# Optimization experiments

Measured on AMD Instinct MI355X. Metric: run time of the kernel, lower is better.

Reference implementation:

```python
import jax, jax.numpy as jnp
import numpy as np

B, S, HID = 4, 1024, 1024
NH, HD = 16, 64  # num heads, head dim


def setup_inputs() -> dict:
    key = jax.random.key(0)
    ks = jax.random.split(key, 8)
    scale = 0.02
    return {
        "hidden_states": jax.random.normal(ks[0], (B, S, HID), dtype=jnp.float32),
        "attention_mask": jnp.ones((B, 1, 1, S), dtype=jnp.float32),
        "Wq": jax.random.normal(ks[1], (HID, HID), dtype=jnp.float32) * scale,
        "bq": jnp.zeros((HID,), dtype=jnp.float32),
        "Wk": jax.random.normal(ks[2], (HID, HID), dtype=jnp.float32) * scale,
        "bk": jnp.zeros((HID,), dtype=jnp.float32),
        "Wv": jax.random.normal(ks[3], (HID, HID), dtype=jnp.float32) * scale,
        "bv": jnp.zeros((HID,), dtype=jnp.float32),
    }


def reference(hidden_states, attention_mask, Wq, bq, Wk, bk, Wv, bv):
    # Linear projections: torch nn.Linear computes x @ W.T + b
    q = hidden_states @ Wq.T + bq  # [B,S,HID]
    k = hidden_states @ Wk.T + bk
    v = hidden_states @ Wv.T + bv

    def split_heads(x):
        return x.reshape(B, S, NH, HD).transpose(0, 2, 1, 3)  # [B,NH,S,HD]

    q, k, v = split_heads(q), split_heads(k), split_heads(v)

    scores = jnp.einsum("bhqd,bhkd->bhqk", q, k) / jnp.sqrt(jnp.float32(HD))
    # faithful to original: scores - (2 - mask) * 1e6
    scores = scores - (2.0 - attention_mask) * 1.0e6
    probs = jax.nn.softmax(scores, axis=-1)
    # dropout: eval mode -> identity
    ctx = jnp.einsum("bhqk,bhkd->bhqd", probs, v)  # [B,NH,S,HD]
    ctx = ctx.transpose(0, 2, 1, 3).reshape(B, S, HID)
    return ctx
```

## Files before the change

### kernel.cpp

```cpp
#include <hip/hip_runtime.h>
#include <math.h>

#define B_ 4
#define S_ 1024
#define HID_ 1024
#define NH_ 16
#define HD_ 64
#define NTOK (B_ * S_)

typedef __attribute__((ext_vector_type(4))) float f32x4;
typedef __attribute__((ext_vector_type(8))) short bf16x8;

__device__ __forceinline__ unsigned short f2bf(float f) {
    union { float f; unsigned int u; } v; v.f = f;
    unsigned int r = v.u + 0x7fffu + ((v.u >> 16) & 1u);
    return (unsigned short)(r >> 16);
}

#if __has_builtin(__builtin_amdgcn_cvt_pk_bf16_f32)
__device__ __forceinline__ unsigned int pk_bf16(float a, float b) {
    auto v = __builtin_amdgcn_cvt_pk_bf16_f32(a, b);
    union { decltype(v) v; unsigned int u; } cv; cv.v = v;
    return cv.u;
}
#else
__device__ __forceinline__ unsigned int pk_bf16(float a, float b) {
    return (unsigned int)f2bf(a) | ((unsigned int)f2bf(b) << 16);
}
#endif

__device__ __forceinline__ void load_lds16(const void* g, void* l) {
    __builtin_amdgcn_global_load_lds(
        (const __attribute__((address_space(1))) unsigned int*)(uintptr_t)g,
        (__attribute__((address_space(3))) unsigned int*)(uintptr_t)l,
        16, 0, 0);
}

__global__ __launch_bounds__(256) void cvt_all(
    const float* __restrict__ x, const float* __restrict__ wq,
    const float* __restrict__ wk, const float* __restrict__ wv,
    unsigned short* __restrict__ xb, unsigned short* __restrict__ wqb,
    unsigned short* __restrict__ wkb, unsigned short* __restrict__ wvb)
{
    const int which = blockIdx.y;
    const float* src = which == 0 ? x : which == 1 ? wq : which == 2 ? wk : wv;
    unsigned short* dst = which == 0 ? xb : which == 1 ? wqb : which == 2 ? wkb : wvb;
    const int n4 = (which == 0) ? (NTOK * HID_ / 4) : (HID_ * HID_ / 4);
    int i = blockIdx.x * 256 + threadIdx.x;
    if (i < n4) {
        float4 f = ((const float4*)src)[i];
        uint2 o;
        o.x = pk_bf16(f.x, f.y);
        o.y = pk_bf16(f.z, f.w);
        ((uint2*)dst)[i] = o;
    }
}

__global__ __launch_bounds__(512, 6) void qkv_gemm_mfma(
    const unsigned short* __restrict__ xb,
    const unsigned short* __restrict__ Wqb, const float* __restrict__ bq,
    const unsigned short* __restrict__ Wkb, const float* __restrict__ bk,
    const unsigned short* __restrict__ Wvb, const float* __restrict__ bv,
    unsigned short* __restrict__ qout, unsigned short* __restrict__ kout,
    unsigned short* __restrict__ vtout)
{
    const int which = blockIdx.z;
    const unsigned short* __restrict__ W = which == 0 ? Wqb : which == 1 ? Wkb : Wvb;
    const float* __restrict__ bias       = which == 0 ? bq  : which == 1 ? bk  : bv;

    __shared__ unsigned short As[128 * 64];
    __shared__ unsigned short Bs[128 * 64];

    const int t    = threadIdx.x;
    const int lane = t & 63;
    const int w    = t >> 6;
    const int wr   = w >> 2;
    const int wc   = w & 3;
    const int g    = lane >> 4;
    const int lrow = lane & 15;

    const int bm = blockIdx.x;
    const int bn = blockIdx.y;

    const unsigned short* __restrict__ Arow = (which == 2) ? W  : xb;
    const unsigned short* __restrict__ Brow = (which == 2) ? xb : W;
    const int am0 = (which == 2) ? bn * 128 : bm * 128;
    const int bn0 = (which == 2) ? bm * 128 : bn * 128;

    const int srow = t >> 3;
    const int sc   = ((t & 7) ^ ((t >> 3) & 7)) << 3;
    const unsigned short* gA = Arow + (size_t)(am0 + srow) * HID_ + sc;
    const unsigned short* gB = Brow + (size_t)(bn0 + srow) * HID_ + sc;

    const f32x4 zero = {0.f, 0.f, 0.f, 0.f};
    f32x4 acc[4][2];
    #pragma unroll
    for (int i = 0; i < 4; ++i)
        #pragma unroll
        for (int j = 0; j < 2; ++j) acc[i][j] = zero;

    for (int k0 = 0; k0 < HID_; k0 += 64) {
        __syncthreads();
        #pragma unroll
        for (int i = 0; i < 2; ++i) {
            load_lds16(gA + (size_t)(i * 64) * HID_ + k0, (char*)As + i * 8192 + t * 16);
            load_lds16(gB + (size_t)(i * 64) * HID_ + k0, (char*)Bs + i * 8192 + t * 16);
        }
        __syncthreads();

        #pragma unroll
        for (int ks = 0; ks < 2; ++ks) {
            bf16x8 af[4], bf[2];
            #pragma unroll
            for (int i = 0; i < 4; ++i) {
                const int row = wr * 64 + i * 16 + lrow;
                af[i] = *(const bf16x8*)&As[row * 64 + (((ks * 4 + g) ^ (row & 7)) << 3)];
            }
            #pragma unroll
            for (int j = 0; j < 2; ++j) {
                const int row = wc * 32 + j * 16 + lrow;
                bf[j] = *(const bf16x8*)&Bs[row * 64 + (((ks * 4 + g) ^ (row & 7)) << 3)];
            }
            #pragma unroll
            for (int i = 0; i < 4; ++i)
                #pragma unroll
                for (int j = 0; j < 2; ++j)
                    acc[i][j] = __builtin_amdgcn_mfma_f32_16x16x32_bf16(
                        af[i], bf[j], acc[i][j], 0, 0, 0);
        }
    }

    const int col   = lane & 15;
    const int rbase = (lane >> 4) << 2;
    if (which == 2) {
        #pragma unroll
        for (int i = 0; i < 4; ++i) {
            #pragma unroll
            for (int r = 0; r < 4; ++r) {
                const int feat = bn * 128 + wr * 64 + i * 16 + rbase + r;
                const int h = feat >> 6, d = feat & 63;
                const float bias_v = bias[feat];
                #pragma unroll
                for (int j = 0; j < 2; ++j) {
                    const int tok = bm * 128 + wc * 32 + j * 16 + col;
                    const int b = tok >> 10, s = tok & 1023;
                    vtout[((size_t)((b << 4) + h) << 16) + ((size_t)d << 10) + s] =
                        f2bf(acc[i][j][r] + bias_v);
                }
            }
        }
    } else {
        #pragma unroll
        for (int j = 0; j < 2; ++j) {
            const int feat = bn * 128 + wc * 32 + j * 16 + col;
            const int h = feat >> 6, d = feat & 63;
            const float bias_v = bias[feat];
            #pragma unroll
            for (int i = 0; i < 4; ++i) {
                const int tok0 = bm * 128 + wr * 64 + i * 16 + rbase;
                #pragma unroll
                for (int r = 0; r < 4; ++r) {
                    const int tok = tok0 + r;
                    const int b = tok >> 10, s = tok & 1023;
                    const size_t off = ((size_t)((b << 4) + h) << 16) + ((size_t)s << 6) + d;
                    const float val = acc[i][j][r] + bias_v;
                    if (which == 0) qout[off] = f2bf(val);
                    else            kout[off] = f2bf(val);
                }
            }
        }
    }
}

__global__ __launch_bounds__(512, 4) void attn_mfma(
    const unsigned short* __restrict__ Q, const unsigned short* __restrict__ K,
    const unsigned short* __restrict__ Vt, const float* __restrict__ mask,
    float* __restrict__ out)
{
    __shared__ unsigned short Ks[2][64 * 64];
    __shared__ unsigned short Vts[2][64 * 64];
    __shared__ unsigned short Ps[8][16 * 72];
    __shared__ float Mts[1024];
    __shared__ float Ls[8][16];

    const int t    = threadIdx.x;
    const int lane = t & 63;
    const int w    = t >> 6;
    const int g    = lane >> 4;
    const int ln   = lane & 15;

    const int bh = blockIdx.x;
    const int b  = bh >> 4;
    const int h  = bh & 15;
    const int q0 = blockIdx.y << 7;

    const unsigned short* __restrict__ qg = Q  + ((size_t)bh << 16);
    const unsigned short* __restrict__ kg = K  + ((size_t)bh << 16);
    const unsigned short* __restrict__ vg = Vt + ((size_t)bh << 16);

    const int qrow = w * 16 + ln;

    bf16x8 qreg[2];
    #pragma unroll
    for (int ks = 0; ks < 2; ++ks)
        qreg[ks] = *(const bf16x8*)&qg[(size_t)(q0 + qrow) * 64 + ks * 32 + (g << 3)];

    int fro[2][4];
    #pragma unroll
    for (int ks = 0; ks < 2; ++ks)
        #pragma unroll
        for (int j = 0; j < 4; ++j) {
            const int row = j * 16 + ln;
            fro[ks][j] = (row * 64 + (((ks * 4 + g) ^ (row & 7)) << 3)) * 2;
        }

    const int srow = t >> 3;
    const int scol = ((t & 7) ^ (srow & 7)) << 3;
    const unsigned short* kst = kg + (size_t)srow * 64 + scol;
    const unsigned short* vst = vg + (size_t)srow * 1024 + scol;

    const f32x4 zero = {0.f, 0.f, 0.f, 0.f};
    f32x4 O[4];
    #pragma unroll
    for (int j = 0; j < 4; ++j) O[j] = zero;
    float lacc = 0.f;

    load_lds16(kst, (char*)Ks[0] + t * 16);
    load_lds16(vst, (char*)Vts[0] + t * 16);
    #pragma unroll
    for (int i = 0; i < 2; ++i) {
        const int key = t + i * 512;
        Mts[key] = (2.0f - mask[(b << 10) + key]) * 1.0e6f;
    }
    __syncthreads();

    for (int kt = 0; kt < 16; ++kt) {
        const int cur = kt & 1;

        if (kt < 15) {
            load_lds16(kst + (size_t)(kt + 1) * 4096, (char*)Ks[cur ^ 1] + t * 16);
            load_lds16(vst + (size_t)(kt + 1) * 64,  (char*)Vts[cur ^ 1] + t * 16);
        }

        const unsigned short* Kb = Ks[cur];
        const unsigned short* Vb = Vts[cur];

        f32x4 sacc[4];
        #pragma unroll
        for (int j = 0; j < 4; ++j) sacc[j] = zero;
        {
            bf16x8 kf[2][4];
            #pragma unroll
            for (int ks = 0; ks < 2; ++ks)
                #pragma unroll
                for (int j = 0; j < 4; ++j)
                    kf[ks][j] = *(const bf16x8*)((const char*)Kb + fro[ks][j]);
            __builtin_amdgcn_s_setprio(1);
            #pragma unroll
            for (int ks = 0; ks < 2; ++ks)
                #pragma unroll
                for (int j = 0; j < 4; ++j)
                    sacc[j] = __builtin_amdgcn_mfma_f32_16x16x32_bf16(
                        kf[ks][j], qreg[ks], sacc[j], 0, 0, 0);
            __builtin_amdgcn_s_setprio(0);
        }

        #pragma unroll
        for (int j = 0; j < 4; ++j) {
            const f32x4 m4 = *(const f32x4*)&Mts[kt * 64 + j * 16 + (g << 2)];
            float p[4];
            #pragma unroll
            for (int r = 0; r < 4; ++r) {
                const float sv = sacc[j][r] * 0.125f - m4[r];
                p[r] = __expf(sv + 1.0e6f);
            }
            lacc += (p[0] + p[1]) + (p[2] + p[3]);
            uint2 pk;
            pk.x = pk_bf16(p[0], p[1]);
            pk.y = pk_bf16(p[2], p[3]);
            *(uint2*)&Ps[w][ln * 72 + j * 16 + (g << 2)] = pk;
        }
        asm volatile("s_waitcnt lgkmcnt(0)" ::: "memory");

        {
            bf16x8 pf[2], vf[2][4];
            #pragma unroll
            for (int ks = 0; ks < 2; ++ks) {
                pf[ks] = *(const bf16x8*)&Ps[w][ln * 72 + ks * 32 + (g << 3)];
                #pragma unroll
                for (int j = 0; j < 4; ++j)
                    vf[ks][j] = *(const bf16x8*)((const char*)Vb + fro[ks][j]);
            }
            __builtin_amdgcn_s_setprio(1);
            #pragma unroll
            for (int ks = 0; ks < 2; ++ks)
                #pragma unroll
                for (int j = 0; j < 4; ++j)
                    O[j] = __builtin_amdgcn_mfma_f32_16x16x32_bf16(
                        pf[ks], vf[ks][j], O[j], 0, 0, 0);
            __builtin_amdgcn_s_setprio(0);
        }

        __syncthreads();
    }

    float rs = lacc;
    rs += __shfl_xor(rs, 16);
    rs += __shfl_xor(rs, 32);
    if (lane < 16) Ls[w][ln] = rs;
    asm volatile("s_waitcnt lgkmcnt(0)" ::: "memory");
    #pragma unroll
    for (int r = 0; r < 4; ++r) {
        const float inv = 1.0f / Ls[w][(g << 2) + r];
        const int q = q0 + w * 16 + (g << 2) + r;
        const size_t base = (((size_t)(b << 10) + q) << 10) + (h << 6);
        #pragma unroll
        for (int j = 0; j < 4; ++j)
            out[base + j * 16 + ln] = O[j][r] * inv;
    }
}

extern "C" void kernel_launch(void* const* d_in, const int* in_sizes, int n_in,
                              void* d_out, int out_size, void* d_ws, size_t ws_size,
                              hipStream_t stream) {
    const float* hs   = (const float*)d_in[0];
    const float* mask = (const float*)d_in[1];
    const float* Wq   = (const float*)d_in[2];
    const float* bq   = (const float*)d_in[3];
    const float* Wk   = (const float*)d_in[4];
    const float* bk   = (const float*)d_in[5];
    const float* Wv   = (const float*)d_in[6];
    const float* bv   = (const float*)d_in[7];
    float* out = (float*)d_out;

    char* ws = (char*)d_ws;
    unsigned short* xb  = (unsigned short*)(ws);
    unsigned short* wqb = (unsigned short*)(ws + ((size_t)8  << 20));
    unsigned short* wkb = (unsigned short*)(ws + ((size_t)10 << 20));
    unsigned short* wvb = (unsigned short*)(ws + ((size_t)12 << 20));
    unsigned short* qb  = (unsigned short*)(ws + ((size_t)14 << 20));
    unsigned short* kb  = (unsigned short*)(ws + ((size_t)22 << 20));
    unsigned short* vtb = (unsigned short*)(ws + ((size_t)30 << 20));

    cvt_all<<<dim3(4096, 4), 256, 0, stream>>>(hs, Wq, Wk, Wv, xb, wqb, wkb, wvb);
    qkv_gemm_mfma<<<dim3(NTOK / 128, HID_ / 128, 3), 512, 0, stream>>>(
        xb, wqb, bq, wkb, bk, wvb, bv, qb, kb, vtb);
    attn_mfma<<<dim3(B_ * NH_, S_ / 128), 512, 0, stream>>>(qb, kb, vtb, mask, out);
}
```

Before: 148.1 us.

## Switch attention to 32x32x16 MFMA with register-resident P via permlane swaps

```diff
diff --git a/kernel.cpp b/kernel.cpp
--- a/kernel.cpp
+++ b/kernel.cpp
@@ -9,6 +9,7 @@
 #define NTOK (B_ * S_)
 
 typedef __attribute__((ext_vector_type(4))) float f32x4;
+typedef __attribute__((ext_vector_type(16))) float f32x16;
 typedef __attribute__((ext_vector_type(8))) short bf16x8;
 
 __device__ __forceinline__ unsigned short f2bf(float f) {
@@ -26,6 +27,23 @@
 #else
 __device__ __forceinline__ unsigned int pk_bf16(float a, float b) {
     return (unsigned int)f2bf(a) | ((unsigned int)f2bf(b) << 16);
+}
+#endif
+
+#if __has_builtin(__builtin_amdgcn_permlane32_swap)
+__device__ __forceinline__ void plswap(unsigned &a, unsigned &b) {
+    typedef __attribute__((ext_vector_type(2))) int v2i;
+    v2i r = __builtin_amdgcn_permlane32_swap((int)a, (int)b, false, false);
+    a = (unsigned)r[0]; b = (unsigned)r[1];
+}
+#else
+__device__ __forceinline__ void plswap(unsigned &a, unsigned &b) {
+    const unsigned bl = __shfl_xor(b, 32);
+    const unsigned ah = __shfl_xor(a, 32);
+    const bool hi = ((threadIdx.x & 63) >> 5) != 0;
+    const unsigned na = hi ? bl : a;
+    const unsigned nb = hi ? b  : ah;
+    a = na; b = nb;
 }
 #endif
 
@@ -172,64 +190,62 @@
     }
 }
 
-__global__ __launch_bounds__(512, 4) void attn_mfma(
+__global__ __launch_bounds__(256, 2) void attn_mfma(
     const unsigned short* __restrict__ Q, const unsigned short* __restrict__ K,
     const unsigned short* __restrict__ Vt, const float* __restrict__ mask,
     float* __restrict__ out)
 {
     __shared__ unsigned short Ks[2][64 * 64];
     __shared__ unsigned short Vts[2][64 * 64];
-    __shared__ unsigned short Ps[8][16 * 72];
     __shared__ float Mts[1024];
-    __shared__ float Ls[8][16];
+    __shared__ float Ls[4][32];
 
     const int t    = threadIdx.x;
     const int lane = t & 63;
     const int w    = t >> 6;
-    const int g    = lane >> 4;
-    const int ln   = lane & 15;
+    const int q31  = lane & 31;
+    const int hl   = lane >> 5;
 
     const int bh = blockIdx.x;
     const int b  = bh >> 4;
     const int h  = bh & 15;
-    const int q0 = blockIdx.y << 7;
+    const int q0w = (blockIdx.y << 7) + (w << 5);
 
     const unsigned short* __restrict__ qg = Q  + ((size_t)bh << 16);
     const unsigned short* __restrict__ kg = K  + ((size_t)bh << 16);
     const unsigned short* __restrict__ vg = Vt + ((size_t)bh << 16);
 
-    const int qrow = w * 16 + ln;
-
-    bf16x8 qreg[2];
-    #pragma unroll
-    for (int ks = 0; ks < 2; ++ks)
-        qreg[ks] = *(const bf16x8*)&qg[(size_t)(q0 + qrow) * 64 + ks * 32 + (g << 3)];
-
-    int fro[2][4];
-    #pragma unroll
-    for (int ks = 0; ks < 2; ++ks)
-        #pragma unroll
-        for (int j = 0; j < 4; ++j) {
-            const int row = j * 16 + ln;
-            fro[ks][j] = (row * 64 + (((ks * 4 + g) ^ (row & 7)) << 3)) * 2;
-        }
+    bf16x8 qreg[4];
+    {
+        const unsigned short* qp = qg + ((size_t)(q0w + q31) << 6);
+        #pragma unroll
+        for (int kc = 0; kc < 4; ++kc)
+            qreg[kc] = *(const bf16x8*)&qp[kc * 16 + (hl << 3)];
+    }
+
+    int fro[4];
+    #pragma unroll
+    for (int kc = 0; kc < 4; ++kc)
+        fro[kc] = q31 * 128 + ((((kc << 1) + hl) ^ (q31 & 7)) << 4);
 
     const int srow = t >> 3;
-    const int scol = ((t & 7) ^ (srow & 7)) << 3;
-    const unsigned short* kst = kg + (size_t)srow * 64 + scol;
-    const unsigned short* vst = vg + (size_t)srow * 1024 + scol;
-
-    const f32x4 zero = {0.f, 0.f, 0.f, 0.f};
-    f32x4 O[4];
-    #pragma unroll
-    for (int j = 0; j < 4; ++j) O[j] = zero;
+    const int c8   = ((t & 7) ^ (srow & 7)) << 3;
+    const unsigned short* kst = kg + (size_t)srow * 64 + c8;
+    const unsigned short* vst = vg + (size_t)srow * 1024 + c8;
+
+    f32x16 O[2];
+    #pragma unroll
+    for (int i = 0; i < 16; ++i) { O[0][i] = 0.f; O[1][i] = 0.f; }
     float lacc = 0.f;
 
-    load_lds16(kst, (char*)Ks[0] + t * 16);
-    load_lds16(vst, (char*)Vts[0] + t * 16);
     #pragma unroll
     for (int i = 0; i < 2; ++i) {
-        const int key = t + i * 512;
+        load_lds16(kst + i * 2048,  (char*)Ks[0]  + i * 4096 + t * 16);
+        load_lds16(vst + i * 32768, (char*)Vts[0] + i * 4096 + t * 16);
+    }
+    #pragma unroll
+    for (int i = 0; i < 4; ++i) {
+        const int key = t + i * 256;
         Mts[key] = (2.0f - mask[(b << 10) + key]) * 1.0e6f;
     }
     __syncthreads();
@@ -238,85 +254,91 @@
         const int cur = kt & 1;
 
         if (kt < 15) {
-            load_lds16(kst + (size_t)(kt + 1) * 4096, (char*)Ks[cur ^ 1] + t * 16);
-            load_lds16(vst + (size_t)(kt + 1) * 64,  (char*)Vts[cur ^ 1] + t * 16);
-        }
-
-        const unsigned short* Kb = Ks[cur];
-        const unsigned short* Vb = Vts[cur];
-
-        f32x4 sacc[4];
-        #pragma unroll
-        for (int j = 0; j < 4; ++j) sacc[j] = zero;
-        {
-            bf16x8 kf[2][4];
-            #pragma unroll
-            for (int ks = 0; ks < 2; ++ks)
+            #pragma unroll
+            for (int i = 0; i < 2; ++i) {
+                load_lds16(kst + i * 2048 + (size_t)(kt + 1) * 4096,
+                           (char*)Ks[cur ^ 1] + i * 4096 + t * 16);
+                load_lds16(vst + i * 32768 + (size_t)(kt + 1) * 64,
+                           (char*)Vts[cur ^ 1] + i * 4096 + t * 16);
+            }
+        }
+
+        const char* Kb = (const char*)Ks[cur];
+        const char* Vb = (const char*)Vts[cur];
+
+        f32x16 sacc[2];
+        #pragma unroll
+        for (int i = 0; i < 16; ++i) { sacc[0][i] = 0.f; sacc[1][i] = 0.f; }
+        #pragma unroll
+        for (int kb = 0; kb < 2; ++kb) {
+            bf16x8 kf[4];
+            #pragma unroll
+            for (int kc = 0; kc < 4; ++kc)
+                kf[kc] = *(const bf16x8*)(Kb + kb * 4096 + fro[kc]);
+            __builtin_amdgcn_s_setprio(1);
+            #pragma unroll
+            for (int kc = 0; kc < 4; ++kc)
+                sacc[kb] = __builtin_amdgcn_mfma_f32_32x32x16_bf16(
+                    kf[kc], qreg[kc], sacc[kb], 0, 0, 0);
+            __builtin_amdgcn_s_setprio(0);
+        }
+
+        bf16x8 pf[4];
+        #pragma unroll
+        for (int kb = 0; kb < 2; ++kb) {
+            unsigned u[4][2];
+            #pragma unroll
+            for (int rq = 0; rq < 4; ++rq) {
+                const f32x4 m4 = *(const f32x4*)&Mts[kt * 64 + kb * 32 + rq * 8 + (hl << 2)];
+                float p[4];
                 #pragma unroll
-                for (int j = 0; j < 4; ++j)
-                    kf[ks][j] = *(const bf16x8*)((const char*)Kb + fro[ks][j]);
+                for (int r = 0; r < 4; ++r) {
+                    const float sv = sacc[kb][rq * 4 + r] * 0.125f - m4[r];
+                    p[r] = __expf(sv + 1.0e6f);
+                }
+                lacc += (p[0] + p[1]) + (p[2] + p[3]);
+                u[rq][0] = pk_bf16(p[0], p[1]);
+                u[rq][1] = pk_bf16(p[2], p[3]);
+            }
+            #pragma unroll
+            for (int c = 0; c < 2; ++c) {
+                unsigned w0 = u[2 * c][0], w2 = u[2 * c + 1][0];
+                plswap(w0, w2);
+                unsigned w1 = u[2 * c][1], w3 = u[2 * c + 1][1];
+                plswap(w1, w3);
+                union { unsigned u[4]; bf16x8 v; } f;
+                f.u[0] = w0; f.u[1] = w1; f.u[2] = w2; f.u[3] = w3;
+                pf[kb * 2 + c] = f.v;
+            }
+        }
+
+        #pragma unroll
+        for (int hb = 0; hb < 2; ++hb) {
+            bf16x8 vf[4];
+            #pragma unroll
+            for (int kc = 0; kc < 4; ++kc)
+                vf[kc] = *(const bf16x8*)(Vb + hb * 4096 + fro[kc]);
             __builtin_amdgcn_s_setprio(1);
             #pragma unroll
-            for (int ks = 0; ks < 2; ++ks)
-                #pragma unroll
-                for (int j = 0; j < 4; ++j)
-                    sacc[j] = __builtin_amdgcn_mfma_f32_16x16x32_bf16(
-                        kf[ks][j], qreg[ks], sacc[j], 0, 0, 0);
+            for (int kc = 0; kc < 4; ++kc)
+                O[hb] = __builtin_amdgcn_mfma_f32_32x32x16_bf16(
+                    pf[kc], vf[kc], O[hb], 0, 0, 0);
             __builtin_amdgcn_s_setprio(0);
         }
 
-        #pragma unroll
-        for (int j = 0; j < 4; ++j) {
-            const f32x4 m4 = *(const f32x4*)&Mts[kt * 64 + j * 16 + (g << 2)];
-            float p[4];
-            #pragma unroll
-            for (int r = 0; r < 4; ++r) {
-                const float sv = sacc[j][r] * 0.125f - m4[r];
-                p[r] = __expf(sv + 1.0e6f);
-            }
-            lacc += (p[0] + p[1]) + (p[2] + p[3]);
-            uint2 pk;
-            pk.x = pk_bf16(p[0], p[1]);
-            pk.y = pk_bf16(p[2], p[3]);
-            *(uint2*)&Ps[w][ln * 72 + j * 16 + (g << 2)] = pk;
-        }
-        asm volatile("s_waitcnt lgkmcnt(0)" ::: "memory");
-
-        {
-            bf16x8 pf[2], vf[2][4];
-            #pragma unroll
-            for (int ks = 0; ks < 2; ++ks) {
-                pf[ks] = *(const bf16x8*)&Ps[w][ln * 72 + ks * 32 + (g << 3)];
-                #pragma unroll
-                for (int j = 0; j < 4; ++j)
-                    vf[ks][j] = *(const bf16x8*)((const char*)Vb + fro[ks][j]);
-            }
-            __builtin_amdgcn_s_setprio(1);
-            #pragma unroll
-            for (int ks = 0; ks < 2; ++ks)
-                #pragma unroll
-                for (int j = 0; j < 4; ++j)
-                    O[j] = __builtin_amdgcn_mfma_f32_16x16x32_bf16(
-                        pf[ks], vf[ks][j], O[j], 0, 0, 0);
-            __builtin_amdgcn_s_setprio(0);
-        }
-
         __syncthreads();
     }
 
-    float rs = lacc;
-    rs += __shfl_xor(rs, 16);
-    rs += __shfl_xor(rs, 32);
-    if (lane < 16) Ls[w][ln] = rs;
+    const float l = lacc + __shfl_xor(lacc, 32);
+    if (lane < 32) Ls[w][q31] = l;
     asm volatile("s_waitcnt lgkmcnt(0)" ::: "memory");
     #pragma unroll
-    for (int r = 0; r < 4; ++r) {
-        const float inv = 1.0f / Ls[w][(g << 2) + r];
-        const int q = q0 + w * 16 + (g << 2) + r;
-        const size_t base = (((size_t)(b << 10) + q) << 10) + (h << 6);
-        #pragma unroll
-        for (int j = 0; j < 4; ++j)
-            out[base + j * 16 + ln] = O[j][r] * inv;
+    for (int r = 0; r < 16; ++r) {
+        const int qr = (r & 3) + ((r >> 2) << 3) + (hl << 2);
+        const float inv = 1.0f / Ls[w][qr];
+        const size_t base = (((size_t)(b << 10) + (q0w + qr)) << 10) + (h << 6);
+        out[base + q31]      = O[0][r] * inv;
+        out[base + 32 + q31] = O[1][r] * inv;
     }
 }
 
@@ -345,5 +367,5 @@
     cvt_all<<<dim3(4096, 4), 256, 0, stream>>>(hs, Wq, Wk, Wv, xb, wqb, wkb, wvb);
     qkv_gemm_mfma<<<dim3(NTOK / 128, HID_ / 128, 3), 512, 0, stream>>>(
         xb, wqb, bq, wkb, bk, wvb, bv, qb, kb, vtb);
-    attn_mfma<<<dim3(B_ * NH_, S_ / 128), 512, 0, stream>>>(qb, kb, vtb, mask, out);
-}
+    attn_mfma<<<dim3(B_ * NH_, S_ / 128), 256, 0, stream>>>(qb, kb, vtb, mask, out);
+}
```

After: 150.4 us. Within noise of the previous version (+1.5%).
